# Performance work log

Measured on AMD Instinct MI355X. Metric: run time of the kernel, lower is better.

Reference implementation:

```python
import jax, jax.numpy as jnp
import numpy as np

FREQ = 129  # STFT_FILTERS // 2


def conv1d(x, w, b, stride, pad):
    # x: [B, Cin, L], w: [Cout, Cin, K] (torch Conv1d layout)
    out = jax.lax.conv_general_dilated(x, w, (stride,), [(pad, pad)],
                                       dimension_numbers=('NCH', 'OIH', 'NCH'))
    if b is not None:
        out = out + b[None, :, None]
    return out


def setup_inputs() -> dict:
    key = jax.random.key(0)
    ks = jax.random.split(key, 17)
    B = 16384
    s = 0.05
    return {
        'x': jax.random.normal(ks[0], (B, 512), jnp.float32),
        'state': jax.random.normal(ks[1], (2, B, 128), jnp.float32),
        'stft_w': jax.random.normal(ks[2], (258, 1, 256), jnp.float32) * s,
        'w1': jax.random.normal(ks[3], (128, 129, 3), jnp.float32) * s,
        'b1': jax.random.normal(ks[4], (128,), jnp.float32) * s,
        'w2': jax.random.normal(ks[5], (64, 128, 3), jnp.float32) * s,
        'b2': jax.random.normal(ks[6], (64,), jnp.float32) * s,
        'w3': jax.random.normal(ks[7], (64, 64, 3), jnp.float32) * s,
        'b3': jax.random.normal(ks[8], (64,), jnp.float32) * s,
        'w4': jax.random.normal(ks[9], (128, 64, 3), jnp.float32) * s,
        'b4': jax.random.normal(ks[10], (128,), jnp.float32) * s,
        'w_ih': jax.random.normal(ks[11], (512, 128), jnp.float32) * s,
        'w_hh': jax.random.normal(ks[12], (512, 128), jnp.float32) * s,
        'b_ih': jax.random.normal(ks[13], (512,), jnp.float32) * s,
        'b_hh': jax.random.normal(ks[14], (512,), jnp.float32) * s,
        'fw': jax.random.normal(ks[15], (1, 128, 1), jnp.float32) * s,
        'fb': jax.random.normal(ks[16], (1,), jnp.float32) * s,
    }


def reference(x, state, stft_w, w1, b1, w2, b2, w3, b3, w4, b4,
              w_ih, w_hh, b_ih, b_hh, fw, fb):
    # reflect-pad right by 64: [B, 512] -> [B, 576], add channel dim
    xp = jnp.pad(x, ((0, 0), (0, 64)), mode='reflect')[:, None, :]
    s = conv1d(xp, stft_w, None, 128, 0)            # [B, 258, 3]
    real, imag = s[:, :FREQ], s[:, FREQ:]
    h = jnp.sqrt(real * real + imag * imag)          # magnitude [B, 129, 3]
    h = jax.nn.relu(conv1d(h, w1, b1, 1, 1))         # [B, 128, 3]
    h = jax.nn.relu(conv1d(h, w2, b2, 2, 1))         # [B, 64, 2]
    h = jax.nn.relu(conv1d(h, w3, b3, 2, 1))         # [B, 64, 1]
    h = jax.nn.relu(conv1d(h, w4, b4, 1, 1))         # [B, 128, 1]
    feat = h[:, :, 0]                                # [B, 128]
    # torch LSTMCell: gate order i, f, g, o
    gates = feat @ w_ih.T + b_ih + state[0] @ w_hh.T + b_hh
    i, f, g, o = jnp.split(gates, 4, axis=1)
    c = jax.nn.sigmoid(f) * state[1] + jax.nn.sigmoid(i) * jnp.tanh(g)
    hn = jax.nn.sigmoid(o) * jnp.tanh(c)
    new_state = jnp.stack([hn, c], axis=0)           # [2, B, 128]
    z = jax.nn.relu(hn)[:, :, None]                  # [B, 128, 1]
    z = jax.nn.sigmoid(conv1d(z, fw, fb, 1, 0))      # [B, 1, 1]
    out = z[:, 0].mean(axis=1, keepdims=True)        # [B, 1]
    return out, new_state
```

## Files before the change

kernel.cpp:

```cpp
#include <hip/hip_runtime.h>
#include <math.h>

typedef unsigned short ushort_t;
typedef short short8 __attribute__((ext_vector_type(8)));
typedef float floatx4 __attribute__((ext_vector_type(4)));

#define MFMA16(a,b,c) __builtin_amdgcn_mfma_f32_16x16x32_bf16((a),(b),(c),0,0,0)

#define PK_STFT 0
#define PK_W1   69632
#define PK_W2   131072
#define PK_W3   155648
#define PK_W4   167936
#define PK_LSTM 176128
#define OFF_MAG 307200
#define OFF_FEAT 8171520

__device__ __forceinline__ ushort_t f2bf(float f){
    unsigned int u = __float_as_uint(f);
    u += 0x7fffu + ((u >> 16) & 1u);
    return (ushort_t)(u >> 16);
}
__device__ __forceinline__ float bf2f(ushort_t h){
    return __uint_as_float(((unsigned int)h) << 16);
}
__device__ __forceinline__ unsigned int pack2(float a, float b){
    return (unsigned int)f2bf(a) | ((unsigned int)f2bf(b) << 16);
}
__device__ __forceinline__ float fsig(float v){
    return __builtin_amdgcn_rcpf(1.f + __builtin_amdgcn_exp2f(-1.44269504f * v));
}
__device__ __forceinline__ float ftanh(float v){
    return 2.f * __builtin_amdgcn_rcpf(1.f + __builtin_amdgcn_exp2f(-2.88539008f * v)) - 1.f;
}

__global__ __launch_bounds__(256) void prep_kernel(
    const float* __restrict__ stft_w, const float* __restrict__ w1,
    const float* __restrict__ w2, const float* __restrict__ w3,
    const float* __restrict__ w4, const float* __restrict__ wih,
    const float* __restrict__ whh, ushort_t* __restrict__ wp)
{
    int i = blockIdx.x * 256 + threadIdx.x;
    if (i >= 307200) return;
    float val = 0.f;
    if (i < PK_W1) {
        int frag = i >> 9, rr = i & 511, l = rr >> 3, j = rr & 7;
        int ct = frag >> 3, kk = frag & 7;
        int kd = kk * 32 + ((l >> 4) << 3) + j;
        int n = ct * 16 + (l & 15);
        val = (n < 258) ? stft_w[n * 256 + kd] : 0.f;
    } else if (i < PK_W2) {
        int r = i - PK_W1;
        int tap = r / 20480; r -= tap * 20480;
        int frag = r >> 9, rr = r & 511, l = rr >> 3, j = rr & 7;
        int ct = frag / 5, kk = frag - ct * 5;
        int kd = kk * 32 + ((l >> 4) << 3) + j;
        int c = ct * 16 + (l & 15);
        val = (kd < 129) ? w1[c * 387 + kd * 3 + tap] : 0.f;
    } else if (i < PK_W3) {
        int r = i - PK_W2;
        int frag = r >> 9, rr = r & 511, l = rr >> 3, j = rr & 7;
        int ct = frag / 12, kk = frag - ct * 12;
        int kd = kk * 32 + ((l >> 4) << 3) + j;
        int k = kd >> 7, f = kd & 127;
        int c = ct * 16 + (l & 15);
        val = w2[c * 384 + f * 3 + k];
    } else if (i < PK_W4) {
        int r = i - PK_W3;
        int frag = r >> 9, rr = r & 511, l = rr >> 3, j = rr & 7;
        int ct = frag / 6, kk = frag - ct * 6;
        int kd = kk * 32 + ((l >> 4) << 3) + j;
        int k = kd >> 6, f = kd & 63;
        int c = ct * 16 + (l & 15);
        val = w3[c * 192 + f * 3 + k];
    } else if (i < PK_LSTM) {
        int r = i - PK_W4;
        int frag = r >> 9, rr = r & 511, l = rr >> 3, j = rr & 7;
        int ct = frag >> 1, kk = frag & 1;
        int kd = kk * 32 + ((l >> 4) << 3) + j;
        int c = ct * 16 + (l & 15);
        val = w4[c * 192 + kd * 3 + 1];
    } else {
        int r = i - PK_LSTM;
        int frag = r >> 9, rr = r & 511, l = rr >> 3, j = rr & 7;
        int ct = frag >> 3, kk = frag & 7;
        int kd = kk * 32 + ((l >> 4) << 3) + j;
        int n = ct * 16 + (l & 15);
        val = (kd < 128) ? wih[n * 128 + kd] : whh[n * 128 + (kd - 128)];
    }
    wp[i] = f2bf(val);
}

__global__ __launch_bounds__(256, 3) void stft_kernel(
    const float* __restrict__ x, const ushort_t* __restrict__ wp,
    ushort_t* __restrict__ magg)
{
    __shared__ ushort_t xs[48 * 264];
    __shared__ ushort_t s[48 * 264];
    const int tid = threadIdx.x, lane = tid & 63, wid = tid >> 6;
    const int l15 = lane & 15, lk = lane >> 4;

    {
        const float4* xg = (const float4*)(x + (size_t)blockIdx.x * 16 * 512);
#pragma unroll
        for (int i = 0; i < 8; ++i) {
            int idx4 = tid + i * 256;
            float4 v = xg[idx4];
            int b = idx4 >> 7, c4 = idx4 & 127;
            int si = c4 * 4, t1 = si >> 7;
            unsigned int u0 = pack2(v.x, v.y), u1 = pack2(v.z, v.w);
            if (t1 < 3) {
                ushort_t* p = &xs[(b * 3 + t1) * 264 + (si & 127)];
                *(unsigned int*)p = u0; *(unsigned int*)(p + 2) = u1;
            }
            if (t1 >= 1) {
                ushort_t* p = &xs[(b * 3 + t1 - 1) * 264 + (si & 127) + 128];
                *(unsigned int*)p = u0; *(unsigned int*)(p + 2) = u1;
            }
        }
    }
    __syncthreads();

    for (int ct = wid; ct < 17; ct += 4) {
        short8 bfrag[8];
        const short8* bp = (const short8*)(wp + PK_STFT) + (size_t)(ct * 8) * 64 + lane;
#pragma unroll
        for (int kk = 0; kk < 8; ++kk) bfrag[kk] = bp[kk * 64];
        int col = ct * 16 + l15;
#pragma unroll
        for (int rt = 0; rt < 3; ++rt) {
            const ushort_t* abase = &xs[(rt * 16 + l15) * 264 + lk * 8];
            floatx4 acc = {0.f, 0.f, 0.f, 0.f};
#pragma unroll
            for (int kk = 0; kk < 8; ++kk) {
                short8 af = *(const short8*)(abase + kk * 32);
                acc = MFMA16(af, bfrag[kk], acc);
            }
            if (col < 258) {
                int r0 = rt * 16 + lk * 4;
#pragma unroll
                for (int jj = 0; jj < 4; ++jj) s[(r0 + jj) * 264 + col] = f2bf(acc[jj]);
            }
        }
    }
    __syncthreads();

    {
        ushort_t* ml = xs;
        for (int idx = tid; idx < 48 * 129; idx += 256) {
            int bt = idx / 129, f = idx - bt * 129;
            float re = bf2f(s[bt * 264 + f]);
            float im = bf2f(s[bt * 264 + 129 + f]);
            int b = bt / 3, t = bt - b * 3;
            ml[b * 480 + t * 160 + f] = f2bf(sqrtf(re * re + im * im));
        }
        for (int idx = tid; idx < 48 * 31; idx += 256) {
            int bt = idx / 31, f = 129 + (idx - bt * 31);
            int b = bt / 3, t = bt - b * 3;
            ml[b * 480 + t * 160 + f] = 0;
        }
    }
    __syncthreads();
    {
        unsigned int* mgd = (unsigned int*)(magg + (size_t)blockIdx.x * 16 * 480);
        const unsigned int* mls = (const unsigned int*)xs;
#pragma unroll
        for (int k = 0; k < 15; ++k) mgd[tid + k * 256] = mls[tid + k * 256];
    }
}

__global__ __launch_bounds__(256) void conv_kernel(
    const ushort_t* __restrict__ wp, const ushort_t* __restrict__ magg,
    const float* __restrict__ b1, const float* __restrict__ b2,
    const float* __restrict__ b3, const float* __restrict__ b4,
    ushort_t* __restrict__ featg)
{
    __shared__ ushort_t big[13440];
    __shared__ ushort_t h2h[16 * 3 * 72];
    __shared__ ushort_t h3s[16 * 72];
    const int tid = threadIdx.x, lane = tid & 63, wid = tid >> 6;
    const int l15 = lane & 15, lk = lane >> 4;

    {
        unsigned int* bz = (unsigned int*)big;
        for (int i = tid; i < 2688; i += 256) {
            int bb = i / 168, r = i - bb * 168;
            int tp = (r < 84) ? 0 : 4, f2 = (r < 84) ? r : r - 84;
            bz[(bb * 5 + tp) * 84 + f2] = 0u;
        }
        for (int i = tid; i < 576; i += 256) {
            int bb = i / 36, f2 = i - bb * 36;
            ((unsigned int*)h2h)[bb * 108 + f2] = 0u;
        }
        const unsigned int* mg = (const unsigned int*)(magg + (size_t)blockIdx.x * 16 * 480);
        for (int i = tid; i < 3840; i += 256) {
            int bb = i / 240, r = i - bb * 240;
            int t = r / 80, f2 = r - t * 80;
            bz[(bb * 5 + 1 + t) * 84 + f2] = mg[i];
        }
    }
    __syncthreads();

    floatx4 acc1[2][3];
#pragma unroll
    for (int ci = 0; ci < 2; ++ci)
#pragma unroll
        for (int rt = 0; rt < 3; ++rt) acc1[ci][rt] = (floatx4){0.f, 0.f, 0.f, 0.f};
#pragma unroll
    for (int ci = 0; ci < 2; ++ci) {
        int ct = wid + ci * 4;
        short8 bfrag[15];
#pragma unroll
        for (int tap = 0; tap < 3; ++tap)
#pragma unroll
            for (int kk = 0; kk < 5; ++kk)
                bfrag[tap * 5 + kk] = ((const short8*)(wp + PK_W1))[(size_t)(tap * 40 + ct * 5 + kk) * 64 + lane];
#pragma unroll
        for (int rt = 0; rt < 3; ++rt) {
            int obt = rt * 16 + l15;
            int b = obt / 3, t = obt - b * 3;
#pragma unroll
            for (int tap = 0; tap < 3; ++tap) {
                const ushort_t* abase = &big[(b * 5 + t + tap) * 168 + lk * 8];
#pragma unroll
                for (int kk = 0; kk < 5; ++kk) {
                    short8 af = *(const short8*)(abase + kk * 32);
                    acc1[ci][rt] = MFMA16(af, bfrag[tap * 5 + kk], acc1[ci][rt]);
                }
            }
        }
    }
    __syncthreads();

    {
        unsigned int* h1z = (unsigned int*)big;
        for (int i = tid; i < 2176; i += 256) {
            int bb = i / 136, r = i - bb * 136;
            int tp = (r < 68) ? 0 : 4, f2 = (r < 68) ? r : r - 68;
            h1z[(bb * 5 + tp) * 68 + f2] = 0u;
        }
#pragma unroll
        for (int ci = 0; ci < 2; ++ci) {
            int ct = wid + ci * 4;
            int col = ct * 16 + l15;
            float bias = b1[col];
#pragma unroll
            for (int rt = 0; rt < 3; ++rt)
#pragma unroll
                for (int jj = 0; jj < 4; ++jj) {
                    int obt = rt * 16 + lk * 4 + jj;
                    int b = obt / 3, t = obt - b * 3;
                    big[(b * 5 + t + 1) * 136 + col] = f2bf(fmaxf(acc1[ci][rt][jj] + bias, 0.f));
                }
        }
    }
    __syncthreads();

    {
        int ct = wid;
        short8 bfrag[12];
#pragma unroll
        for (int kk = 0; kk < 12; ++kk)
            bfrag[kk] = ((const short8*)(wp + PK_W2))[(size_t)(ct * 12 + kk) * 64 + lane];
        int col = ct * 16 + l15;
        float bias = b2[col];
#pragma unroll
        for (int rt = 0; rt < 2; ++rt) {
            floatx4 acc = {0.f, 0.f, 0.f, 0.f};
            int orow = rt * 16 + l15;
            int b = orow >> 1, t2 = orow & 1;
#pragma unroll
            for (int kk = 0; kk < 12; ++kk) {
                int k = kk >> 2, f = (kk & 3) * 32 + lk * 8;
                short8 af = *(const short8*)(&big[(b * 5 + 2 * t2 + k) * 136 + f]);
                acc = MFMA16(af, bfrag[kk], acc);
            }
#pragma unroll
            for (int jj = 0; jj < 4; ++jj) {
                int orw = rt * 16 + lk * 4 + jj;
                int bb = orw >> 1, tt = orw & 1;
                h2h[(bb * 3 + 1 + tt) * 72 + col] = f2bf(fmaxf(acc[jj] + bias, 0.f));
            }
        }
    }
    __syncthreads();

    {
        int ct = wid;
        short8 bfrag[6];
#pragma unroll
        for (int kk = 0; kk < 6; ++kk)
            bfrag[kk] = ((const short8*)(wp + PK_W3))[(size_t)(ct * 6 + kk) * 64 + lane];
        int col = ct * 16 + l15;
        float bias = b3[col];
        floatx4 acc = {0.f, 0.f, 0.f, 0.f};
        int b = l15;
#pragma unroll
        for (int kk = 0; kk < 6; ++kk) {
            int k = kk >> 1, f = (kk & 1) * 32 + lk * 8;
            short8 af = *(const short8*)(&h2h[(b * 3 + k) * 72 + f]);
            acc = MFMA16(af, bfrag[kk], acc);
        }
#pragma unroll
        for (int jj = 0; jj < 4; ++jj) {
            int bb = lk * 4 + jj;
            h3s[bb * 72 + col] = f2bf(fmaxf(acc[jj] + bias, 0.f));
        }
    }
    __syncthreads();

    {
        ushort_t* fbuf = h2h;
#pragma unroll
        for (int ci = 0; ci < 2; ++ci) {
            int ct = wid + ci * 4;
            short8 bf0 = ((const short8*)(wp + PK_W4))[(size_t)(ct * 2 + 0) * 64 + lane];
            short8 bf1 = ((const short8*)(wp + PK_W4))[(size_t)(ct * 2 + 1) * 64 + lane];
            int col = ct * 16 + l15;
            float bias = b4[col];
            floatx4 acc = {0.f, 0.f, 0.f, 0.f};
            int b = l15;
            short8 a0 = *(const short8*)(&h3s[b * 72 + lk * 8]);
            short8 a1 = *(const short8*)(&h3s[b * 72 + 32 + lk * 8]);
            acc = MFMA16(a0, bf0, acc);
            acc = MFMA16(a1, bf1, acc);
#pragma unroll
            for (int jj = 0; jj < 4; ++jj) {
                int bb = lk * 4 + jj;
                fbuf[bb * 128 + col] = f2bf(fmaxf(acc[jj] + bias, 0.f));
            }
        }
        __syncthreads();
        unsigned int* fgd = (unsigned int*)(featg + (size_t)blockIdx.x * 16 * 128);
        const unsigned int* fls = (const unsigned int*)fbuf;
#pragma unroll
        for (int k = 0; k < 4; ++k) fgd[tid + k * 256] = fls[tid + k * 256];
    }
}

__global__ __launch_bounds__(512, 6) void lstm_kernel(
    const ushort_t* __restrict__ featg, const float* __restrict__ state,
    const ushort_t* __restrict__ wp, const float* __restrict__ bih,
    const float* __restrict__ bhh, const float* __restrict__ fw,
    const float* __restrict__ fbp, float* __restrict__ out, int B)
{
    __shared__ ushort_t inc[32 * 264];
    __shared__ float cpl[32 * 132];
    __shared__ float red[256];
    const int tid = threadIdx.x, lane = tid & 63, wid = tid >> 6;
    const int l15 = lane & 15, lk = lane >> 4;
    const size_t b0 = (size_t)blockIdx.x * 32;
    const int cc = wid * 16 + l15;
    const float* cprev = state + (size_t)B * 128;

    {
        const unsigned int* fg = (const unsigned int*)(featg + b0 * 128);
        unsigned int* ip = (unsigned int*)inc;
        for (int i = tid; i < 2048; i += 512) {
            int bb = i >> 6, f2 = i & 63;
            ip[bb * 132 + f2] = fg[i];
        }
        const float2* hp2 = (const float2*)(state + b0 * 128);
        for (int i = tid; i < 2048; i += 512) {
            int bb = i >> 6, c2 = i & 63;
            float2 v = hp2[i];
            ip[bb * 132 + 64 + c2] = pack2(v.x, v.y);
        }
        const float* cg = cprev + b0 * 128;
        for (int i = tid; i < 4096; i += 512) {
            int bb = i >> 7, c = i & 127;
            cpl[bb * 132 + c] = cg[i];
        }
    }
    __syncthreads();

    floatx4 acc[4][2];
#pragma unroll
    for (int ci = 0; ci < 4; ++ci) {
        int ct = wid + ci * 8;
        short8 bfrag[8];
#pragma unroll
        for (int kk = 0; kk < 8; ++kk)
            bfrag[kk] = ((const short8*)(wp + PK_LSTM))[(size_t)(ct * 8 + kk) * 64 + lane];
#pragma unroll
        for (int rt = 0; rt < 2; ++rt) {
            const ushort_t* abase = &inc[(rt * 16 + l15) * 264 + lk * 8];
            floatx4 a = {0.f, 0.f, 0.f, 0.f};
#pragma unroll
            for (int kk = 0; kk < 8; ++kk) {
                short8 af = *(const short8*)(abase + kk * 32);
                a = MFMA16(af, bfrag[kk], a);
            }
            acc[ci][rt] = a;
        }
    }
    __syncthreads();

    float* hsl = (float*)inc;
    float* csl = cpl;
    const float bi = bih[cc] + bhh[cc];
    const float bf_ = bih[cc + 128] + bhh[cc + 128];
    const float bg = bih[cc + 256] + bhh[cc + 256];
    const float bo = bih[cc + 384] + bhh[cc + 384];
    const float fwv = fw[cc];
    float ph[2][4];
#pragma unroll
    for (int rt = 0; rt < 2; ++rt)
#pragma unroll
        for (int jj = 0; jj < 4; ++jj) {
            int row = rt * 16 + lk * 4 + jj;
            float gi = acc[0][rt][jj] + bi;
            float gf = acc[1][rt][jj] + bf_;
            float gg = acc[2][rt][jj] + bg;
            float go = acc[3][rt][jj] + bo;
            float cn = fsig(gf) * cpl[row * 132 + cc] + fsig(gi) * ftanh(gg);
            float hn = fsig(go) * ftanh(cn);
            hsl[row * 132 + cc] = hn;
            csl[row * 132 + cc] = cn;
            ph[rt][jj] = fmaxf(hn, 0.f) * fwv;
        }

#pragma unroll
    for (int rt = 0; rt < 2; ++rt)
#pragma unroll
        for (int jj = 0; jj < 4; ++jj) {
            float v = ph[rt][jj];
            v += __shfl_xor(v, 1, 64);
            v += __shfl_xor(v, 2, 64);
            v += __shfl_xor(v, 4, 64);
            v += __shfl_xor(v, 8, 64);
            if (l15 == 0) red[wid * 32 + rt * 16 + lk * 4 + jj] = v;
        }
    __syncthreads();

    {
        float* outh = out + B + b0 * 128;
        float* outc = out + B + (size_t)B * 128 + b0 * 128;
        for (int i = tid; i < 4096; i += 512) {
            int bb = i >> 7, c = i & 127;
            outh[i] = hsl[bb * 132 + c];
            outc[i] = csl[bb * 132 + c];
        }
    }
    if (tid < 32) {
        float v = 0.f;
#pragma unroll
        for (int w = 0; w < 8; ++w) v += red[w * 32 + tid];
        out[b0 + tid] = fsig(v + fbp[0]);
    }
}

extern "C" void kernel_launch(void* const* d_in, const int* in_sizes, int n_in,
                              void* d_out, int out_size, void* d_ws, size_t ws_size,
                              hipStream_t stream) {
    const float* x      = (const float*)d_in[0];
    const float* state  = (const float*)d_in[1];
    const float* stft_w = (const float*)d_in[2];
    const float* w1     = (const float*)d_in[3];
    const float* b1     = (const float*)d_in[4];
    const float* w2     = (const float*)d_in[5];
    const float* b2     = (const float*)d_in[6];
    const float* w3     = (const float*)d_in[7];
    const float* b3     = (const float*)d_in[8];
    const float* w4     = (const float*)d_in[9];
    const float* b4     = (const float*)d_in[10];
    const float* wih    = (const float*)d_in[11];
    const float* whh    = (const float*)d_in[12];
    const float* bih    = (const float*)d_in[13];
    const float* bhh    = (const float*)d_in[14];
    const float* fw     = (const float*)d_in[15];
    const float* fbp    = (const float*)d_in[16];

    ushort_t* wp = (ushort_t*)d_ws;
    const int B = in_sizes[0] / 512;

    prep_kernel<<<1200, 256, 0, stream>>>(stft_w, w1, w2, w3, w4, wih, whh, wp);
    stft_kernel<<<B / 16, 256, 0, stream>>>(x, wp, wp + OFF_MAG);
    conv_kernel<<<B / 16, 256, 0, stream>>>(wp, wp + OFF_MAG, b1, b2, b3, b4, wp + OFF_FEAT);
    lstm_kernel<<<B / 32, 512, 0, stream>>>(wp + OFF_FEAT, state, wp, bih, bhh, fw, fbp,
                                            (float*)d_out, B);
}
```

Before: 80.78 us.

## Fuse STFT magnitude and conv stack into a single feature kernel

Merges the STFT kernel and the conv kernel into one kernel, so the bf16 magnitude tensor stays in shared memory instead of going through global memory. This removes a global write and read of about 16 KB per block group plus one kernel launch. STFT accumulators for all column tiles are now held in registers across a barrier so the input buffer can be reused for the results, which raises register pressure. The kernel keeps launch bounds of 3 blocks per CU with about 52 KB of shared memory per block.

```diff
diff --git a/kernel.cpp b/kernel.cpp
--- a/kernel.cpp
+++ b/kernel.cpp
@@ -13,8 +13,7 @@
 #define PK_W3   155648
 #define PK_W4   167936
 #define PK_LSTM 176128
-#define OFF_MAG 307200
-#define OFF_FEAT 8171520
+#define OFF_FEAT 307200
 
 __device__ __forceinline__ ushort_t f2bf(float f){
     unsigned int u = __float_as_uint(f);
@@ -91,17 +90,22 @@
     wp[i] = f2bf(val);
 }
 
-__global__ __launch_bounds__(256, 3) void stft_kernel(
+__global__ __launch_bounds__(256, 3) void feat_kernel(
     const float* __restrict__ x, const ushort_t* __restrict__ wp,
-    ushort_t* __restrict__ magg)
+    const float* __restrict__ b1, const float* __restrict__ b2,
+    const float* __restrict__ b3, const float* __restrict__ b4,
+    ushort_t* __restrict__ featg)
 {
-    __shared__ ushort_t xs[48 * 264];
-    __shared__ ushort_t s[48 * 264];
+    __shared__ ushort_t A[12672];
+    __shared__ ushort_t Bb[13440];
+
     const int tid = threadIdx.x, lane = tid & 63, wid = tid >> 6;
     const int l15 = lane & 15, lk = lane >> 4;
-
-    {
-        const float4* xg = (const float4*)(x + (size_t)blockIdx.x * 16 * 512);
+    const size_t b0 = (size_t)blockIdx.x * 16;
+
+    for (int i = tid; i < 6720; i += 256) ((unsigned int*)Bb)[i] = 0u;
+    {
+        const float4* xg = (const float4*)(x + b0 * 512);
 #pragma unroll
         for (int i = 0; i < 8; ++i) {
             int idx4 = tid + i * 256;
@@ -110,94 +114,67 @@
             int si = c4 * 4, t1 = si >> 7;
             unsigned int u0 = pack2(v.x, v.y), u1 = pack2(v.z, v.w);
             if (t1 < 3) {
-                ushort_t* p = &xs[(b * 3 + t1) * 264 + (si & 127)];
+                ushort_t* p = &A[(b * 3 + t1) * 264 + (si & 127)];
                 *(unsigned int*)p = u0; *(unsigned int*)(p + 2) = u1;
             }
             if (t1 >= 1) {
-                ushort_t* p = &xs[(b * 3 + t1 - 1) * 264 + (si & 127) + 128];
+                ushort_t* p = &A[(b * 3 + t1 - 1) * 264 + (si & 127) + 128];
                 *(unsigned int*)p = u0; *(unsigned int*)(p + 2) = u1;
             }
         }
     }
     __syncthreads();
 
-    for (int ct = wid; ct < 17; ct += 4) {
-        short8 bfrag[8];
-        const short8* bp = (const short8*)(wp + PK_STFT) + (size_t)(ct * 8) * 64 + lane;
-#pragma unroll
-        for (int kk = 0; kk < 8; ++kk) bfrag[kk] = bp[kk * 64];
-        int col = ct * 16 + l15;
-#pragma unroll
-        for (int rt = 0; rt < 3; ++rt) {
-            const ushort_t* abase = &xs[(rt * 16 + l15) * 264 + lk * 8];
-            floatx4 acc = {0.f, 0.f, 0.f, 0.f};
-#pragma unroll
-            for (int kk = 0; kk < 8; ++kk) {
-                short8 af = *(const short8*)(abase + kk * 32);
-                acc = MFMA16(af, bfrag[kk], acc);
-            }
+    floatx4 accs[5][3];
+#pragma unroll
+    for (int ci = 0; ci < 5; ++ci)
+#pragma unroll
+        for (int rt = 0; rt < 3; ++rt) accs[ci][rt] = (floatx4){0.f, 0.f, 0.f, 0.f};
+#pragma unroll
+    for (int ci = 0; ci < 5; ++ci) {
+        int ct = wid + ci * 4;
+        if (ct < 17) {
+            short8 bfrag[8];
+            const short8* bp = (const short8*)(wp + PK_STFT) + (size_t)(ct * 8) * 64 + lane;
+#pragma unroll
+            for (int kk = 0; kk < 8; ++kk) bfrag[kk] = bp[kk * 64];
+#pragma unroll
+            for (int rt = 0; rt < 3; ++rt) {
+                const ushort_t* abase = &A[(rt * 16 + l15) * 264 + lk * 8];
+                floatx4 a = accs[ci][rt];
+#pragma unroll
+                for (int kk = 0; kk < 8; ++kk)
+                    a = MFMA16(*(const short8*)(abase + kk * 32), bfrag[kk], a);
+                accs[ci][rt] = a;
+            }
+        }
+    }
+    __syncthreads();
+
+#pragma unroll
+    for (int ci = 0; ci < 5; ++ci) {
+        int ct = wid + ci * 4;
+        if (ct < 17) {
+            int col = ct * 16 + l15;
             if (col < 258) {
-                int r0 = rt * 16 + lk * 4;
-#pragma unroll
-                for (int jj = 0; jj < 4; ++jj) s[(r0 + jj) * 264 + col] = f2bf(acc[jj]);
-            }
-        }
-    }
-    __syncthreads();
-
-    {
-        ushort_t* ml = xs;
-        for (int idx = tid; idx < 48 * 129; idx += 256) {
-            int bt = idx / 129, f = idx - bt * 129;
-            float re = bf2f(s[bt * 264 + f]);
-            float im = bf2f(s[bt * 264 + 129 + f]);
-            int b = bt / 3, t = bt - b * 3;
-            ml[b * 480 + t * 160 + f] = f2bf(sqrtf(re * re + im * im));
-        }
-        for (int idx = tid; idx < 48 * 31; idx += 256) {
-            int bt = idx / 31, f = 129 + (idx - bt * 31);
-            int b = bt / 3, t = bt - b * 3;
-            ml[b * 480 + t * 160 + f] = 0;
-        }
-    }
-    __syncthreads();
-    {
-        unsigned int* mgd = (unsigned int*)(magg + (size_t)blockIdx.x * 16 * 480);
-        const unsigned int* mls = (const unsigned int*)xs;
-#pragma unroll
-        for (int k = 0; k < 15; ++k) mgd[tid + k * 256] = mls[tid + k * 256];
-    }
-}
-
-__global__ __launch_bounds__(256) void conv_kernel(
-    const ushort_t* __restrict__ wp, const ushort_t* __restrict__ magg,
-    const float* __restrict__ b1, const float* __restrict__ b2,
-    const float* __restrict__ b3, const float* __restrict__ b4,
-    ushort_t* __restrict__ featg)
-{
-    __shared__ ushort_t big[13440];
-    __shared__ ushort_t h2h[16 * 3 * 72];
-    __shared__ ushort_t h3s[16 * 72];
-    const int tid = threadIdx.x, lane = tid & 63, wid = tid >> 6;
-    const int l15 = lane & 15, lk = lane >> 4;
-
-    {
-        unsigned int* bz = (unsigned int*)big;
-        for (int i = tid; i < 2688; i += 256) {
-            int bb = i / 168, r = i - bb * 168;
-            int tp = (r < 84) ? 0 : 4, f2 = (r < 84) ? r : r - 84;
-            bz[(bb * 5 + tp) * 84 + f2] = 0u;
-        }
-        for (int i = tid; i < 576; i += 256) {
-            int bb = i / 36, f2 = i - bb * 36;
-            ((unsigned int*)h2h)[bb * 108 + f2] = 0u;
-        }
-        const unsigned int* mg = (const unsigned int*)(magg + (size_t)blockIdx.x * 16 * 480);
-        for (int i = tid; i < 3840; i += 256) {
-            int bb = i / 240, r = i - bb * 240;
-            int t = r / 80, f2 = r - t * 80;
-            bz[(bb * 5 + 1 + t) * 84 + f2] = mg[i];
-        }
+#pragma unroll
+                for (int rt = 0; rt < 3; ++rt) {
+                    int r0 = rt * 16 + lk * 4;
+#pragma unroll
+                    for (int jj = 0; jj < 4; ++jj)
+                        A[(r0 + jj) * 264 + col] = f2bf(accs[ci][rt][jj]);
+                }
+            }
+        }
+    }
+    __syncthreads();
+
+    for (int idx = tid; idx < 6192; idx += 256) {
+        int bt = idx / 129, f = idx - bt * 129;
+        float re = bf2f(A[bt * 264 + f]);
+        float im = bf2f(A[bt * 264 + 129 + f]);
+        int b = bt / 3, t = bt - b * 3;
+        Bb[b * 840 + (1 + t) * 168 + f] = f2bf(sqrtf(re * re + im * im));
     }
     __syncthreads();
 
@@ -221,28 +198,29 @@
             int b = obt / 3, t = obt - b * 3;
 #pragma unroll
             for (int tap = 0; tap < 3; ++tap) {
-                const ushort_t* abase = &big[(b * 5 + t + tap) * 168 + lk * 8];
-#pragma unroll
-                for (int kk = 0; kk < 5; ++kk) {
-                    short8 af = *(const short8*)(abase + kk * 32);
-                    acc1[ci][rt] = MFMA16(af, bfrag[tap * 5 + kk], acc1[ci][rt]);
-                }
-            }
-        }
-    }
-    __syncthreads();
-
-    {
-        unsigned int* h1z = (unsigned int*)big;
+                const ushort_t* abase = &Bb[(b * 5 + t + tap) * 168 + lk * 8];
+#pragma unroll
+                for (int kk = 0; kk < 5; ++kk)
+                    acc1[ci][rt] = MFMA16(*(const short8*)(abase + kk * 32), bfrag[tap * 5 + kk], acc1[ci][rt]);
+            }
+        }
+    }
+    __syncthreads();
+
+    {
+        unsigned int* h1z = (unsigned int*)A;
         for (int i = tid; i < 2176; i += 256) {
             int bb = i / 136, r = i - bb * 136;
             int tp = (r < 68) ? 0 : 4, f2 = (r < 68) ? r : r - 68;
             h1z[(bb * 5 + tp) * 68 + f2] = 0u;
         }
+        for (int i = tid; i < 576; i += 256) {
+            int bb = i / 36, f2 = i - bb * 36;
+            ((unsigned int*)Bb)[bb * 108 + f2] = 0u;
+        }
 #pragma unroll
         for (int ci = 0; ci < 2; ++ci) {
-            int ct = wid + ci * 4;
-            int col = ct * 16 + l15;
+            int ct = wid + ci * 4, col = ct * 16 + l15;
             float bias = b1[col];
 #pragma unroll
             for (int rt = 0; rt < 3; ++rt)
@@ -250,7 +228,7 @@
                 for (int jj = 0; jj < 4; ++jj) {
                     int obt = rt * 16 + lk * 4 + jj;
                     int b = obt / 3, t = obt - b * 3;
-                    big[(b * 5 + t + 1) * 136 + col] = f2bf(fmaxf(acc1[ci][rt][jj] + bias, 0.f));
+                    A[(b * 5 + t + 1) * 136 + col] = f2bf(fmaxf(acc1[ci][rt][jj] + bias, 0.f));
                 }
         }
     }
@@ -272,14 +250,14 @@
 #pragma unroll
             for (int kk = 0; kk < 12; ++kk) {
                 int k = kk >> 2, f = (kk & 3) * 32 + lk * 8;
-                short8 af = *(const short8*)(&big[(b * 5 + 2 * t2 + k) * 136 + f]);
+                short8 af = *(const short8*)(&A[(b * 5 + 2 * t2 + k) * 136 + f]);
                 acc = MFMA16(af, bfrag[kk], acc);
             }
 #pragma unroll
             for (int jj = 0; jj < 4; ++jj) {
                 int orw = rt * 16 + lk * 4 + jj;
                 int bb = orw >> 1, tt = orw & 1;
-                h2h[(bb * 3 + 1 + tt) * 72 + col] = f2bf(fmaxf(acc[jj] + bias, 0.f));
+                Bb[(bb * 3 + 1 + tt) * 72 + col] = f2bf(fmaxf(acc[jj] + bias, 0.f));
             }
         }
     }
@@ -298,19 +276,17 @@
 #pragma unroll
         for (int kk = 0; kk < 6; ++kk) {
             int k = kk >> 1, f = (kk & 1) * 32 + lk * 8;
-            short8 af = *(const short8*)(&h2h[(b * 3 + k) * 72 + f]);
+            short8 af = *(const short8*)(&Bb[(b * 3 + k) * 72 + f]);
             acc = MFMA16(af, bfrag[kk], acc);
         }
 #pragma unroll
-        for (int jj = 0; jj < 4; ++jj) {
-            int bb = lk * 4 + jj;
-            h3s[bb * 72 + col] = f2bf(fmaxf(acc[jj] + bias, 0.f));
-        }
-    }
-    __syncthreads();
-
-    {
-        ushort_t* fbuf = h2h;
+        for (int jj = 0; jj < 4; ++jj)
+            A[(lk * 4 + jj) * 72 + col] = f2bf(fmaxf(acc[jj] + bias, 0.f));
+    }
+    __syncthreads();
+
+    {
+        ushort_t* fbuf = Bb;
 #pragma unroll
         for (int ci = 0; ci < 2; ++ci) {
             int ct = wid + ci * 4;
@@ -320,18 +296,16 @@
             float bias = b4[col];
             floatx4 acc = {0.f, 0.f, 0.f, 0.f};
             int b = l15;
-            short8 a0 = *(const short8*)(&h3s[b * 72 + lk * 8]);
-            short8 a1 = *(const short8*)(&h3s[b * 72 + 32 + lk * 8]);
+            short8 a0 = *(const short8*)(&A[b * 72 + lk * 8]);
+            short8 a1 = *(const short8*)(&A[b * 72 + 32 + lk * 8]);
             acc = MFMA16(a0, bf0, acc);
             acc = MFMA16(a1, bf1, acc);
 #pragma unroll
-            for (int jj = 0; jj < 4; ++jj) {
-                int bb = lk * 4 + jj;
-                fbuf[bb * 128 + col] = f2bf(fmaxf(acc[jj] + bias, 0.f));
-            }
+            for (int jj = 0; jj < 4; ++jj)
+                fbuf[(lk * 4 + jj) * 128 + col] = f2bf(fmaxf(acc[jj] + bias, 0.f));
         }
         __syncthreads();
-        unsigned int* fgd = (unsigned int*)(featg + (size_t)blockIdx.x * 16 * 128);
+        unsigned int* fgd = (unsigned int*)(featg + b0 * 128);
         const unsigned int* fls = (const unsigned int*)fbuf;
 #pragma unroll
         for (int k = 0; k < 4; ++k) fgd[tid + k * 256] = fls[tid + k * 256];
@@ -475,8 +449,7 @@
     const int B = in_sizes[0] / 512;
 
     prep_kernel<<<1200, 256, 0, stream>>>(stft_w, w1, w2, w3, w4, wih, whh, wp);
-    stft_kernel<<<B / 16, 256, 0, stream>>>(x, wp, wp + OFF_MAG);
-    conv_kernel<<<B / 16, 256, 0, stream>>>(wp, wp + OFF_MAG, b1, b2, b3, b4, wp + OFF_FEAT);
+    feat_kernel<<<B / 16, 256, 0, stream>>>(x, wp, b1, b2, b3, b4, wp + OFF_FEAT);
     lstm_kernel<<<B / 32, 512, 0, stream>>>(wp + OFF_FEAT, state, wp, bih, bhh, fw, fbp,
                                             (float*)d_out, B);
 }
```

New measurement: 92.73 us. 1.15x slower.
